# Kernel optimization log

Hardware: AMD Instinct MI355X
Metric: run time of the kernel (lower is better)

## Reference

```python
import jax, jax.numpy as jnp
import numpy as np

BETA = 0.25
EPS = 1e-10


def setup_inputs() -> dict:
    key = jax.random.key(0)
    k1, k2 = jax.random.split(key)
    x = jax.random.normal(k1, (32, 64, 64, 64), dtype=jnp.float32)  # [B, C=embed_dim, H, W]
    embeddings = jax.random.normal(k2, (64, 512), dtype=jnp.float32)  # [embed_dim, K]
    return {"x": x, "embeddings": embeddings}


def reference(x, embeddings):
    B, C, H, W = x.shape
    K = embeddings.shape[1]
    sg = jax.lax.stop_gradient

    z_e = jnp.transpose(x, (0, 2, 3, 1))          # [B, H, W, C]
    z_flat = z_e.reshape(-1, C)                    # [N, C]

    # Squared L2 distances to codebook: ||z||^2 + ||e||^2 - 2 z.e
    dists = (
        jnp.sum(z_flat * z_flat, axis=1, keepdims=True)
        + jnp.sum(embeddings * embeddings, axis=0)
        - 2.0 * (z_flat @ embeddings)
    )                                              # [N, K]
    idx = jnp.argmin(dists, axis=1)                # [N]

    # Direct gather instead of one-hot matmul (same math)
    quantized = embeddings.T[idx].reshape(z_e.shape)  # [B, H, W, C]

    e_latent_loss = jnp.mean((sg(quantized) - z_e) ** 2)
    q_latent_loss = jnp.mean((quantized - sg(z_e)) ** 2)
    loss = q_latent_loss + BETA * e_latent_loss

    # Straight-through estimator
    quantized_st = z_e + sg(quantized - z_e)

    # Perplexity via codebook usage histogram (== mean of one-hot encodings)
    N = idx.shape[0]
    counts = jnp.zeros((K,), dtype=jnp.float32).at[idx].add(1.0)
    avg_probs = counts / N
    perplexity = jnp.exp(-jnp.sum(avg_probs * jnp.log(avg_probs + EPS)))

    quantized_out = jnp.transpose(quantized_st, (0, 3, 1, 2))  # [B, C, H, W]
    encoding_indices = idx.reshape(B, H, W)
    return loss, quantized_out, perplexity, encoding_indices
```

## Files before the change

### kernel.cpp

```cpp
#include <hip/hip_runtime.h>


#define B_ 32
#define C_ 64
#define HW_ 4096
#define K_ 512
#define N_ (B_ * HW_)
#define NC_ ((long long)N_ * C_)
#define ROWS_ 64
#define NBLK_ (N_ / ROWS_)
#define HBLK_ 64

typedef __attribute__((ext_vector_type(8))) short short8;
typedef __attribute__((ext_vector_type(4))) float float4_t;


__device__ __forceinline__ unsigned short f2bf(float f) {
    unsigned u = __float_as_uint(f);
    u += 0x7fffu + ((u >> 16) & 1u);
    return (unsigned short)(u >> 16);
}
__device__ __forceinline__ float bf2f(unsigned short h) {
    return __uint_as_float(((unsigned)h) << 16);
}
__device__ __forceinline__ int offA(int r, int c) {
    return ((r >> 4) << 10) + ((c >> 3) << 7) + ((r & 15) << 3) + (c & 7);
}
__device__ __forceinline__ void merge2(float& m1, int& i1, float& m2,
                                       float om1, int oi1, float om2) {
    if (om1 < m1) { m2 = fminf(m1, om2); m1 = om1; i1 = oi1; }
    else          { m2 = fminf(m2, om1); }
}

__global__ __launch_bounds__(512) void vq_init(const float* __restrict__ emb,
                                               float* __restrict__ snmax_p,
                                               float* __restrict__ en,
                                               float* __restrict__ embT32,
                                               unsigned short* __restrict__ fBhi,
                                               unsigned short* __restrict__ fBlo) {
    __shared__ float smax[8];
    int k = threadIdx.x;
    if (blockIdx.x < 64) {
        int c = blockIdx.x;
        float e = emb[c * K_ + k];
        embT32[k * C_ + c] = e;
        float s = -2.0f * e;
        unsigned short hi = f2bf(s);
        unsigned short lo = f2bf(s - bf2f(hi));
        int kk   = c >> 5;
        int lane = (((c & 31) >> 3) << 4) + (k & 15);
        int fb   = ((k >> 5) << 2) + (((k >> 4) & 1) << 1) + kk;
        int off  = (fb << 9) + (lane << 3) + (c & 7);
        fBhi[off] = hi;
        fBlo[off] = lo;
    } else {
        float s = 0.f;
#pragma unroll
        for (int c = 0; c < C_; ++c) {
            float e = emb[c * K_ + k];
            s += e * e;
        }
        en[k] = s;
        float m = s;
#pragma unroll
        for (int off = 32; off > 0; off >>= 1)
            m = fmaxf(m, __shfl_down(m, off, 64));
        if ((k & 63) == 0) smax[k >> 6] = m;
        __syncthreads();
        if (k == 0) {
            float mm = smax[0];
#pragma unroll
            for (int w2 = 1; w2 < 8; ++w2) mm = fmaxf(mm, smax[w2]);
            *snmax_p = 4.0f * mm;
        }
    }
}

__global__ __launch_bounds__(256) void vq_argmin(const float* __restrict__ x,
                                                 const float* __restrict__ en_g,
                                                 const float* __restrict__ embT32,
                                                 const unsigned short* __restrict__ fBhi,
                                                 const unsigned short* __restrict__ fBlo,
                                                 const float* __restrict__ snmax_p,
                                                 float* __restrict__ out_q,
                                                 float* __restrict__ out_idx,
                                                 double* __restrict__ ssepart) {
    __shared__ unsigned short Ast[ROWS_ * C_];
    __shared__ float sEn[K_];
    __shared__ float znp[4 * ROWS_];
    __shared__ int   biarr[ROWS_];
    __shared__ int   flaglist[ROWS_];
    __shared__ float wsse[4];
    __shared__ int   nflag;

    const int t   = threadIdx.x;
    const int n0  = blockIdx.x * ROWS_;
    const int b   = n0 >> 12;
    const int hw0 = n0 & 4095;
    const float* xbase = x + ((size_t)b << 18) + hw0;

    if (t == 0) nflag = 0;
    sEn[t]       = en_g[t];
    sEn[256 + t] = en_g[256 + t];

    float v[16];
    float znacc = 0.f;
#pragma unroll
    for (int i = 0; i < 16; ++i) {
        int id = (i << 8) + t;
        int c = id >> 6;
        int r = id & 63;
        float val = xbase[((size_t)c << 12) + r];
        v[i] = val;
        znacc += val * val;
        Ast[offA(r, c)] = f2bf(val);
    }
    znp[((t >> 6) << 6) + (t & 63)] = znacc;
    __syncthreads();

    const int lane = t & 63;
    const int w    = t >> 6;
    const int ln15 = lane & 15;
    const int quad = lane >> 4;
    const float snm = *snmax_p;

    const int ab = (w << 10) + (quad << 7) + (ln15 << 3);
    short8 ah0 = *(const short8*)(Ast + ab);
    short8 ah1 = *(const short8*)(Ast + ab + 512);
    __syncthreads();

#pragma unroll
    for (int i = 0; i < 16; ++i) {
        int id = (i << 8) + t;
        int c = id >> 6;
        int r = id & 63;
        float val = v[i];
        unsigned short hi = f2bf(val);
        Ast[offA(r, c)] = f2bf(val - bf2f(hi));
    }
    __syncthreads();
    short8 al0 = *(const short8*)(Ast + ab);
    short8 al1 = *(const short8*)(Ast + ab + 512);

    float m1[4], m2[4];
    int   i1[4];
#pragma unroll
    for (int reg = 0; reg < 4; ++reg) {
        m1[reg] = 3.4e38f; m2[reg] = 3.4e38f; i1[reg] = 0;
    }

    for (int p = 0; p < 16; ++p) {
#pragma unroll
        for (int ct = 0; ct < 2; ++ct) {
            const int fbase = ((((p << 2) + (ct << 1)) << 9) + (lane << 3));
            short8 bh0 = *(const short8*)(fBhi + fbase);
            short8 bh1 = *(const short8*)(fBhi + fbase + 512);
            short8 bl0 = *(const short8*)(fBlo + fbase);
            short8 bl1 = *(const short8*)(fBlo + fbase + 512);
            float env = sEn[(p << 5) + (ct << 4) + ln15];
            int   idx = (p << 5) + (ct << 4) + ln15;
            float4_t a0 = {0.f, 0.f, 0.f, 0.f};
            float4_t a1 = {0.f, 0.f, 0.f, 0.f};
            a0 = __builtin_amdgcn_mfma_f32_16x16x32_bf16(al0, bh0, a0, 0, 0, 0);
            a1 = __builtin_amdgcn_mfma_f32_16x16x32_bf16(al1, bh1, a1, 0, 0, 0);
            a0 = __builtin_amdgcn_mfma_f32_16x16x32_bf16(ah0, bl0, a0, 0, 0, 0);
            a1 = __builtin_amdgcn_mfma_f32_16x16x32_bf16(ah1, bl1, a1, 0, 0, 0);
            a0 = __builtin_amdgcn_mfma_f32_16x16x32_bf16(ah0, bh0, a0, 0, 0, 0);
            a1 = __builtin_amdgcn_mfma_f32_16x16x32_bf16(ah1, bh1, a1, 0, 0, 0);
#pragma unroll
            for (int reg = 0; reg < 4; ++reg) {
                float vv = (a0[reg] + a1[reg]) + env;
                if (vv < m1[reg]) {
                    m2[reg] = m1[reg]; m1[reg] = vv; i1[reg] = idx;
                } else {
                    m2[reg] = fminf(m2[reg], vv);
                }
            }
        }
    }

#pragma unroll
    for (int reg = 0; reg < 4; ++reg) {
        float a1v = m1[reg], a2v = m2[reg];
        int   ai  = i1[reg];
#pragma unroll
        for (int s = 1; s < 16; s <<= 1) {
            float o1 = __shfl_xor(a1v, s, 16);
            int   oi = __shfl_xor(ai, s, 16);
            float o2 = __shfl_xor(a2v, s, 16);
            merge2(a1v, ai, a2v, o1, oi, o2);
        }
        if (ln15 == 0) {
            int row = (w << 4) + (quad << 2) + reg;
            float znr = znp[row] + znp[64 + row] + znp[128 + row] + znp[192 + row];
            float W = 1.4e-4f * __builtin_sqrtf(znr * snm) + 1e-3f;
            biarr[row] = ai;
            if (a2v > a1v + W) {
                out_idx[n0 + row] = (float)ai;
            } else {
                int pos = atomicAdd(&nflag, 1);
                flaglist[pos] = row;
            }
        }
    }
    __syncthreads();

    int nf = nflag;
    for (int f = w; f < nf; f += 4) {
        int r = flaglist[f];
        float zl = xbase[((size_t)lane << 12) + r];
        float d[8];
#pragma unroll
        for (int j = 0; j < 8; ++j) d[j] = 0.f;
        for (int c4 = 0; c4 < 16; ++c4) {
            float z0 = __shfl(zl, (c4 << 2) + 0, 64);
            float z1 = __shfl(zl, (c4 << 2) + 1, 64);
            float z2 = __shfl(zl, (c4 << 2) + 2, 64);
            float z3 = __shfl(zl, (c4 << 2) + 3, 64);
#pragma unroll
            for (int j = 0; j < 8; ++j) {
                float4_t e = *(const float4_t*)(embT32 + ((((lane << 3) + j) << 6) + (c4 << 2)));
                d[j] = fmaf(z0, e[0], d[j]);
                d[j] = fmaf(z1, e[1], d[j]);
                d[j] = fmaf(z2, e[2], d[j]);
                d[j] = fmaf(z3, e[3], d[j]);
            }
        }
        float znr = znp[r] + znp[64 + r] + znp[128 + r] + znp[192 + r];
        float best = 3.4e38f;
        int   bidx = 0;
#pragma unroll
        for (int j = 0; j < 8; ++j) {
            int k = (lane << 3) + j;
            float dist = (znr + sEn[k]) - 2.f * d[j];
            if (dist < best) { best = dist; bidx = k; }
        }
#pragma unroll
        for (int off = 32; off > 0; off >>= 1) {
            float ov = __shfl_down(best, off, 64);
            int   oi = __shfl_down(bidx, off, 64);
            if (ov < best || (ov == best && oi < bidx)) { best = ov; bidx = oi; }
        }
        if (lane == 0) {
            biarr[r] = bidx;
            out_idx[n0 + r] = (float)bidx;
        }
    }
    __syncthreads();

    const int myrow = (w << 4) + ln15;
    const int code  = biarr[myrow];
    const float* eb = embT32 + (code << 6) + (quad << 3);
    float4_t e0 = *(const float4_t*)(eb);
    float4_t e1 = *(const float4_t*)(eb + 4);
    float4_t e2 = *(const float4_t*)(eb + 32);
    float4_t e3 = *(const float4_t*)(eb + 36);
    float* qrow = out_q + ((size_t)b << 18) + hw0 + myrow;
    float sacc = 0.f;
#pragma unroll
    for (int j = 0; j < 4; ++j) {
        int c0 = (quad << 3) + j;
        int c1 = (quad << 3) + 4 + j;
        float zA = bf2f((unsigned short)ah0[j])     + bf2f((unsigned short)al0[j]);
        float zB = bf2f((unsigned short)ah0[4 + j]) + bf2f((unsigned short)al0[4 + j]);
        float dA = e0[j] - zA, dB = e1[j] - zB;
        sacc += dA * dA + dB * dB;
        qrow[(size_t)c0 << 12] = e0[j];
        qrow[(size_t)c1 << 12] = e1[j];
        float zC = bf2f((unsigned short)ah1[j])     + bf2f((unsigned short)al1[j]);
        float zD = bf2f((unsigned short)ah1[4 + j]) + bf2f((unsigned short)al1[4 + j]);
        float dC = e2[j] - zC, dD = e3[j] - zD;
        sacc += dC * dC + dD * dD;
        qrow[(size_t)(32 + c0) << 12] = e2[j];
        qrow[(size_t)(32 + c1) << 12] = e3[j];
    }
#pragma unroll
    for (int off = 32; off > 0; off >>= 1)
        sacc += __shfl_down(sacc, off, 64);
    if (lane == 0) wsse[w] = sacc;
    __syncthreads();
    if (t == 0)
        ssepart[blockIdx.x] = (double)wsse[0] + (double)wsse[1]
                            + (double)wsse[2] + (double)wsse[3];
}

__global__ __launch_bounds__(256) void vq_hist(const float* __restrict__ out_idx,
                                               int* __restrict__ histpart) {
    __shared__ int h[K_];
    int t = threadIdx.x;
    h[t] = 0; h[t + 256] = 0;
    __syncthreads();
    const float* ip = out_idx + blockIdx.x * (N_ / HBLK_);
#pragma unroll
    for (int i = 0; i < (N_ / HBLK_) / 256; ++i) {
        int k = (int)ip[(i << 8) + t];
        atomicAdd(&h[k], 1);
    }
    __syncthreads();
    histpart[blockIdx.x * K_ + t]       = h[t];
    histpart[blockIdx.x * K_ + 256 + t] = h[t + 256];
}

__global__ __launch_bounds__(512) void vq_final(const int* __restrict__ histpart,
                                                const double* __restrict__ ssepart,
                                                float* __restrict__ out_loss,
                                                float* __restrict__ out_perp) {
    __shared__ float  wsf[8];
    __shared__ double wsd[8];
    int t = threadIdx.x;
    int hsum = 0;
#pragma unroll 8
    for (int b = 0; b < HBLK_; ++b)
        hsum += histpart[b * K_ + t];
    float p = (float)hsum / (float)N_;
    float s = p * logf(p + 1e-10f);
    double d = ssepart[t] + ssepart[t + 512] + ssepart[t + 1024] + ssepart[t + 1536];
#pragma unroll
    for (int off = 32; off > 0; off >>= 1) {
        s += __shfl_down(s, off, 64);
        d += __shfl_down(d, off, 64);
    }
    if ((t & 63) == 0) { wsf[t >> 6] = s; wsd[t >> 6] = d; }
    __syncthreads();
    if (t == 0) {
        float  S = 0.f;
        double D = 0.0;
#pragma unroll
        for (int w = 0; w < 8; ++w) { S += wsf[w]; D += wsd[w]; }
        *out_perp = expf(-S);
        *out_loss = (float)(1.25 * D / (double)NC_);
    }
}

extern "C" void kernel_launch(void* const* d_in, const int* in_sizes, int n_in,
                              void* d_out, int out_size, void* d_ws, size_t ws_size,
                              hipStream_t stream) {
    const float* x   = (const float*)d_in[0];
    const float* emb = (const float*)d_in[1];

    float* out      = (float*)d_out;
    float* out_loss = out;
    float* out_q    = out + 1;
    float* out_perp = out + 1 + (size_t)N_ * C_;
    float* out_idx  = out + 2 + (size_t)N_ * C_;

    char* ws = (char*)d_ws;
    float*          snmax_p  = (float*)(ws + 56);
    float*          en       = (float*)(ws + 2112);
    float*          embT32   = (float*)(ws + 4160);
    unsigned short* fBhi     = (unsigned short*)(ws + 135232);
    unsigned short* fBlo     = (unsigned short*)(ws + 200768);
    int*            histpart = (int*)(ws + 135232);
    double*         ssepart  = (double*)(ws + 266304);

    vq_init<<<65, 512, 0, stream>>>(emb, snmax_p, en, embT32, fBhi, fBlo);
    vq_argmin<<<NBLK_, 256, 0, stream>>>(x, en, embT32, fBhi, fBlo, snmax_p,
                                         out_q, out_idx, ssepart);
    vq_hist<<<HBLK_, 256, 0, stream>>>(out_idx, histpart);
    vq_final<<<1, 512, 0, stream>>>(histpart, ssepart, out_loss, out_perp);
}
```

Measured before the change: 153.6 us.

## Fuse histogram and final reduction into argmin kernel, load MFMA fragments directly

Drops the separate histogram and final kernels. Each argmin block now adds its row codes to a global histogram with atomics, adds its SSE to a double atomic accumulator, and the last block, found through a done counter, computes perplexity and loss. The A-fragment staging through LDS (two writes, two syncs) is replaced by direct per-lane global loads that split each value into hi and lo bf16 parts, folds the codebook norm into the MFMA accumulator's initial value, and makes the top-2 update branchless. This removes two launches and the LDS round trip, at the cost of global atomic contention and less coalesced strided x loads.

```diff
diff --git a/kernel.cpp b/kernel.cpp
--- a/kernel.cpp
+++ b/kernel.cpp
@@ -9,7 +9,6 @@
 #define NC_ ((long long)N_ * C_)
 #define ROWS_ 64
 #define NBLK_ (N_ / ROWS_)
-#define HBLK_ 64
 
 typedef __attribute__((ext_vector_type(8))) short short8;
 typedef __attribute__((ext_vector_type(4))) float float4_t;
@@ -22,9 +21,6 @@
 }
 __device__ __forceinline__ float bf2f(unsigned short h) {
     return __uint_as_float(((unsigned)h) << 16);
-}
-__device__ __forceinline__ int offA(int r, int c) {
-    return ((r >> 4) << 10) + ((c >> 3) << 7) + ((r & 15) << 3) + (c & 7);
 }
 __device__ __forceinline__ void merge2(float& m1, int& i1, float& m2,
                                        float om1, int oi1, float om2) {
@@ -37,7 +33,10 @@
                                                float* __restrict__ en,
                                                float* __restrict__ embT32,
                                                unsigned short* __restrict__ fBhi,
-                                               unsigned short* __restrict__ fBlo) {
+                                               unsigned short* __restrict__ fBlo,
+                                               int* __restrict__ ghist,
+                                               int* __restrict__ done_p,
+                                               double* __restrict__ ssed_p) {
     __shared__ float smax[8];
     int k = threadIdx.x;
     if (blockIdx.x < 64) {
@@ -54,6 +53,8 @@
         fBhi[off] = hi;
         fBlo[off] = lo;
     } else {
+        ghist[k] = 0;
+        if (k == 0) { *done_p = 0; *ssed_p = 0.0; }
         float s = 0.f;
 #pragma unroll
         for (int c = 0; c < C_; ++c) {
@@ -84,63 +85,58 @@
                                                  const float* __restrict__ snmax_p,
                                                  float* __restrict__ out_q,
                                                  float* __restrict__ out_idx,
-                                                 double* __restrict__ ssepart) {
-    __shared__ unsigned short Ast[ROWS_ * C_];
+                                                 int* __restrict__ ghist,
+                                                 double* __restrict__ ssed_p,
+                                                 int* __restrict__ done_p,
+                                                 float* __restrict__ out_loss,
+                                                 float* __restrict__ out_perp) {
     __shared__ float sEn[K_];
-    __shared__ float znp[4 * ROWS_];
+    __shared__ float znrow[ROWS_];
     __shared__ int   biarr[ROWS_];
     __shared__ int   flaglist[ROWS_];
     __shared__ float wsse[4];
     __shared__ int   nflag;
-
-    const int t   = threadIdx.x;
-    const int n0  = blockIdx.x * ROWS_;
-    const int b   = n0 >> 12;
-    const int hw0 = n0 & 4095;
-    const float* xbase = x + ((size_t)b << 18) + hw0;
-
-    if (t == 0) nflag = 0;
-    sEn[t]       = en_g[t];
-    sEn[256 + t] = en_g[256 + t];
-
-    float v[16];
-    float znacc = 0.f;
-#pragma unroll
-    for (int i = 0; i < 16; ++i) {
-        int id = (i << 8) + t;
-        int c = id >> 6;
-        int r = id & 63;
-        float val = xbase[((size_t)c << 12) + r];
-        v[i] = val;
-        znacc += val * val;
-        Ast[offA(r, c)] = f2bf(val);
-    }
-    znp[((t >> 6) << 6) + (t & 63)] = znacc;
-    __syncthreads();
-
+    __shared__ int   amLast;
+
+    const int t    = threadIdx.x;
     const int lane = t & 63;
     const int w    = t >> 6;
     const int ln15 = lane & 15;
     const int quad = lane >> 4;
+    const int n0   = blockIdx.x * ROWS_;
+    const int b    = n0 >> 12;
+    const int hw0  = n0 & 4095;
+    const float* xbase = x + ((size_t)b << 18) + hw0;
+    const int myrow = (w << 4) + ln15;
+
+    if (t == 0) nflag = 0;
+    sEn[t]       = en_g[t];
+    sEn[256 + t] = en_g[256 + t];
+
+    float v0[8], v1[8];
+#pragma unroll
+    for (int j = 0; j < 8; ++j) {
+        v0[j] = xbase[((size_t)((quad << 3) + j) << 12) + myrow];
+        v1[j] = xbase[((size_t)(32 + (quad << 3) + j) << 12) + myrow];
+    }
+    short8 ah0, al0, ah1, al1;
+    float znacc = 0.f;
+#pragma unroll
+    for (int j = 0; j < 8; ++j) {
+        unsigned short h0 = f2bf(v0[j]);
+        ah0[j] = (short)h0;
+        al0[j] = (short)f2bf(v0[j] - bf2f(h0));
+        unsigned short h1 = f2bf(v1[j]);
+        ah1[j] = (short)h1;
+        al1[j] = (short)f2bf(v1[j] - bf2f(h1));
+        znacc += v0[j] * v0[j] + v1[j] * v1[j];
+    }
+    znacc += __shfl_xor(znacc, 16, 64);
+    znacc += __shfl_xor(znacc, 32, 64);
+    if (quad == 0) znrow[myrow] = znacc;
+    __syncthreads();
+
     const float snm = *snmax_p;
-
-    const int ab = (w << 10) + (quad << 7) + (ln15 << 3);
-    short8 ah0 = *(const short8*)(Ast + ab);
-    short8 ah1 = *(const short8*)(Ast + ab + 512);
-    __syncthreads();
-
-#pragma unroll
-    for (int i = 0; i < 16; ++i) {
-        int id = (i << 8) + t;
-        int c = id >> 6;
-        int r = id & 63;
-        float val = v[i];
-        unsigned short hi = f2bf(val);
-        Ast[offA(r, c)] = f2bf(val - bf2f(hi));
-    }
-    __syncthreads();
-    short8 al0 = *(const short8*)(Ast + ab);
-    short8 al1 = *(const short8*)(Ast + ab + 512);
 
     float m1[4], m2[4];
     int   i1[4];
@@ -152,14 +148,15 @@
     for (int p = 0; p < 16; ++p) {
 #pragma unroll
         for (int ct = 0; ct < 2; ++ct) {
+            const int cbase = (p << 5) + (ct << 4);
             const int fbase = ((((p << 2) + (ct << 1)) << 9) + (lane << 3));
             short8 bh0 = *(const short8*)(fBhi + fbase);
             short8 bh1 = *(const short8*)(fBhi + fbase + 512);
             short8 bl0 = *(const short8*)(fBlo + fbase);
             short8 bl1 = *(const short8*)(fBlo + fbase + 512);
-            float env = sEn[(p << 5) + (ct << 4) + ln15];
-            int   idx = (p << 5) + (ct << 4) + ln15;
-            float4_t a0 = {0.f, 0.f, 0.f, 0.f};
+            float env = sEn[cbase + ln15];
+            int   idx = cbase + ln15;
+            float4_t a0 = {env, env, env, env};
             float4_t a1 = {0.f, 0.f, 0.f, 0.f};
             a0 = __builtin_amdgcn_mfma_f32_16x16x32_bf16(al0, bh0, a0, 0, 0, 0);
             a1 = __builtin_amdgcn_mfma_f32_16x16x32_bf16(al1, bh1, a1, 0, 0, 0);
@@ -169,12 +166,12 @@
             a1 = __builtin_amdgcn_mfma_f32_16x16x32_bf16(ah1, bh1, a1, 0, 0, 0);
 #pragma unroll
             for (int reg = 0; reg < 4; ++reg) {
-                float vv = (a0[reg] + a1[reg]) + env;
-                if (vv < m1[reg]) {
-                    m2[reg] = m1[reg]; m1[reg] = vv; i1[reg] = idx;
-                } else {
-                    m2[reg] = fminf(m2[reg], vv);
-                }
+                float vv = a0[reg] + a1[reg];
+                bool  lt = vv < m1[reg];
+                float mx = fmaxf(vv, m1[reg]);
+                m2[reg] = fminf(m2[reg], mx);
+                m1[reg] = fminf(m1[reg], vv);
+                i1[reg] = lt ? idx : i1[reg];
             }
         }
     }
@@ -192,7 +189,7 @@
         }
         if (ln15 == 0) {
             int row = (w << 4) + (quad << 2) + reg;
-            float znr = znp[row] + znp[64 + row] + znp[128 + row] + znp[192 + row];
+            float znr = znrow[row];
             float W = 1.4e-4f * __builtin_sqrtf(znr * snm) + 1e-3f;
             biarr[row] = ai;
             if (a2v > a1v + W) {
@@ -226,7 +223,7 @@
                 d[j] = fmaf(z3, e[3], d[j]);
             }
         }
-        float znr = znp[r] + znp[64 + r] + znp[128 + r] + znp[192 + r];
+        float znr = znrow[r];
         float best = 3.4e38f;
         int   bidx = 0;
 #pragma unroll
@@ -248,7 +245,6 @@
     }
     __syncthreads();
 
-    const int myrow = (w << 4) + ln15;
     const int code  = biarr[myrow];
     const float* eb = embT32 + (code << 6) + (quad << 3);
     float4_t e0 = *(const float4_t*)(eb);
@@ -278,57 +274,36 @@
     for (int off = 32; off > 0; off >>= 1)
         sacc += __shfl_down(sacc, off, 64);
     if (lane == 0) wsse[w] = sacc;
-    __syncthreads();
-    if (t == 0)
-        ssepart[blockIdx.x] = (double)wsse[0] + (double)wsse[1]
-                            + (double)wsse[2] + (double)wsse[3];
-}
-
-__global__ __launch_bounds__(256) void vq_hist(const float* __restrict__ out_idx,
-                                               int* __restrict__ histpart) {
-    __shared__ int h[K_];
-    int t = threadIdx.x;
-    h[t] = 0; h[t + 256] = 0;
-    __syncthreads();
-    const float* ip = out_idx + blockIdx.x * (N_ / HBLK_);
-#pragma unroll
-    for (int i = 0; i < (N_ / HBLK_) / 256; ++i) {
-        int k = (int)ip[(i << 8) + t];
-        atomicAdd(&h[k], 1);
-    }
-    __syncthreads();
-    histpart[blockIdx.x * K_ + t]       = h[t];
-    histpart[blockIdx.x * K_ + 256 + t] = h[t + 256];
-}
-
-__global__ __launch_bounds__(512) void vq_final(const int* __restrict__ histpart,
-                                                const double* __restrict__ ssepart,
-                                                float* __restrict__ out_loss,
-                                                float* __restrict__ out_perp) {
-    __shared__ float  wsf[8];
-    __shared__ double wsd[8];
-    int t = threadIdx.x;
-    int hsum = 0;
-#pragma unroll 8
-    for (int b = 0; b < HBLK_; ++b)
-        hsum += histpart[b * K_ + t];
-    float p = (float)hsum / (float)N_;
-    float s = p * logf(p + 1e-10f);
-    double d = ssepart[t] + ssepart[t + 512] + ssepart[t + 1024] + ssepart[t + 1536];
-#pragma unroll
-    for (int off = 32; off > 0; off >>= 1) {
-        s += __shfl_down(s, off, 64);
-        d += __shfl_down(d, off, 64);
-    }
-    if ((t & 63) == 0) { wsf[t >> 6] = s; wsd[t >> 6] = d; }
-    __syncthreads();
+
+    if (t < ROWS_) atomicAdd(&ghist[biarr[t]], 1);
+    __syncthreads();
+
     if (t == 0) {
-        float  S = 0.f;
-        double D = 0.0;
-#pragma unroll
-        for (int w = 0; w < 8; ++w) { S += wsf[w]; D += wsd[w]; }
-        *out_perp = expf(-S);
-        *out_loss = (float)(1.25 * D / (double)NC_);
+        double bsum = (double)wsse[0] + (double)wsse[1]
+                    + (double)wsse[2] + (double)wsse[3];
+        __hip_atomic_fetch_add(ssed_p, bsum, __ATOMIC_RELAXED, __HIP_MEMORY_SCOPE_AGENT);
+        __threadfence();
+        amLast = (atomicAdd(done_p, 1) == NBLK_ - 1);
+    }
+    __syncthreads();
+    if (amLast) {
+        float s = 0.f;
+        for (int kk = t; kk < K_; kk += 256) {
+            int h = __hip_atomic_load(&ghist[kk], __ATOMIC_RELAXED, __HIP_MEMORY_SCOPE_AGENT);
+            float pp = (float)h * (1.0f / (float)N_);
+            s += pp * logf(pp + 1e-10f);
+        }
+#pragma unroll
+        for (int off = 32; off > 0; off >>= 1)
+            s += __shfl_down(s, off, 64);
+        if (lane == 0) wsse[w] = s;
+        __syncthreads();
+        if (t == 0) {
+            float S = wsse[0] + wsse[1] + wsse[2] + wsse[3];
+            double D = __hip_atomic_load(ssed_p, __ATOMIC_RELAXED, __HIP_MEMORY_SCOPE_AGENT);
+            *out_perp = expf(-S);
+            *out_loss = (float)(1.25 * D / (double)NC_);
+        }
     }
 }
 
@@ -345,17 +320,18 @@
     float* out_idx  = out + 2 + (size_t)N_ * C_;
 
     char* ws = (char*)d_ws;
+    int*            done_p   = (int*)(ws + 0);
+    double*         ssed_p   = (double*)(ws + 8);
     float*          snmax_p  = (float*)(ws + 56);
     float*          en       = (float*)(ws + 2112);
     float*          embT32   = (float*)(ws + 4160);
     unsigned short* fBhi     = (unsigned short*)(ws + 135232);
     unsigned short* fBlo     = (unsigned short*)(ws + 200768);
-    int*            histpart = (int*)(ws + 135232);
-    double*         ssepart  = (double*)(ws + 266304);
-
-    vq_init<<<65, 512, 0, stream>>>(emb, snmax_p, en, embT32, fBhi, fBlo);
+    int*            ghist    = (int*)(ws + 266304);
+
+    vq_init<<<65, 512, 0, stream>>>(emb, snmax_p, en, embT32, fBhi, fBlo,
+                                    ghist, done_p, ssed_p);
     vq_argmin<<<NBLK_, 256, 0, stream>>>(x, en, embT32, fBhi, fBlo, snmax_p,
-                                         out_q, out_idx, ssepart);
-    vq_hist<<<HBLK_, 256, 0, stream>>>(out_idx, histpart);
-    vq_final<<<1, 512, 0, stream>>>(histpart, ssepart, out_loss, out_perp);
-}
+                                         out_q, out_idx, ghist, ssed_p, done_p,
+                                         out_loss, out_perp);
+}
```

Measured after the change: 268.7 us. 74.9% more time.
